# Kernel optimization log

Hardware: AMD Instinct MI355X
Metric: run time of the kernel (lower is better)

The kernel has to match this reference:

```python
import jax, jax.numpy as jnp
import numpy as np

N_NODES = 100000
IN_DIM = 64
OUT_DIM = 64
N_EDGES = 1250000


def setup_inputs() -> dict:
    key = jax.random.key(0)
    k1, k2, k3, k4 = jax.random.split(key, 4)
    x = jax.random.normal(k1, (N_NODES, IN_DIM), dtype=jnp.float32)
    edge_index = jax.random.randint(k2, (2, N_EDGES), 0, N_NODES, dtype=jnp.int32)
    # Linear weights stored as [in, out] so y = x @ W (equivalent to torch x @ W.T)
    s = 1.0 / np.sqrt(IN_DIM)
    W1 = jax.random.uniform(k3, (IN_DIM, OUT_DIM), dtype=jnp.float32, minval=-s, maxval=s)
    W2 = jax.random.uniform(k4, (IN_DIM, OUT_DIM), dtype=jnp.float32, minval=-s, maxval=s)
    return {"x": x, "edge_index": edge_index, "W1": W1, "W2": W2}


def reference(x, edge_index, W1, W2):
    # self part: [N, out]
    self_part = x @ W1
    # transform-then-gather is mathematically identical to gather-then-transform
    # (linear map commutes with row gather) and cheaper when E > N.
    msgs = (x @ W2)[edge_index[0]]            # [E, out]
    neighbor_part = jax.ops.segment_sum(msgs, edge_index[1], num_segments=x.shape[0])
    return jax.nn.relu(self_part + neighbor_part)
```

## Files before the change

### kernel.cpp

```cpp
#include <hip/hip_runtime.h>

#define N_NODES 100000
#define N_EDGES 1250000
#define DIM 64

#define B_SHIFT 7
#define BUCKET_NODES 128
#define NBUCKETS ((N_NODES + BUCKET_NODES - 1) / BUCKET_NODES)
#define CAP 2560
#define P_CHUNK 4096
#define P_THREADS 512
#define NBLK_P ((N_EDGES + P_CHUNK - 1) / P_CHUNK)
#define GEMM_BLOCKS 256
#define SG_THREADS 1024

typedef __attribute__((ext_vector_type(8))) short short8;
typedef __attribute__((ext_vector_type(4))) float f32x4;

static __host__ __device__ inline size_t align256(size_t x) { return (x + 255) & ~(size_t)255; }

__device__ inline float bf16_to_f32(unsigned short u) {
  return __uint_as_float(((unsigned)u) << 16);
}
__device__ inline unsigned short f32_to_bf16(float f) {
  unsigned u = __float_as_uint(f);
  u += 0x7FFFu + ((u >> 16) & 1u);
  return (unsigned short)(u >> 16);
}

__global__ __launch_bounds__(P_THREADS) void fused_gemm_partition(
    const float* __restrict__ x,
    const float* __restrict__ W1,
    const float* __restrict__ W2,
    unsigned short* __restrict__ y1b,
    unsigned short* __restrict__ y2b,
    const int* __restrict__ ei,
    int* __restrict__ gcursor,
    unsigned* __restrict__ pairs,
    int nTiles) {
  __shared__ int h[NBUCKETS];
  __shared__ int scn[NBUCKETS];
  __shared__ int cur[NBUCKETS];
  __shared__ int gbase[NBUCKETS];
  __shared__ int tsum[P_THREADS];
  __shared__ unsigned sval[P_CHUNK];
  __shared__ int saddr[P_CHUNK];

  if (blockIdx.x < NBLK_P) {
    const int nE = N_EDGES;
    int tid = threadIdx.x;
    int base = blockIdx.x * P_CHUNK;
    int end = min(base + P_CHUNK, nE);
    int cntE = end - base;

    for (int i = tid; i < NBUCKETS; i += P_THREADS) h[i] = 0;
    __syncthreads();
    for (int e = base + tid; e < end; e += P_THREADS)
      atomicAdd(&h[ei[nE + e] >> B_SHIFT], 1);
    __syncthreads();

    {
      int b0 = tid * 2;
      int l0 = 0, l1 = 0, s = 0;
      if (b0 < NBUCKETS)     { l0 = s; s += h[b0]; }
      if (b0 + 1 < NBUCKETS) { l1 = s; s += h[b0 + 1]; }
      tsum[tid] = s;
      __syncthreads();
      for (int off = 1; off < P_THREADS; off <<= 1) {
        int t = (tid >= off) ? tsum[tid - off] : 0;
        __syncthreads();
        tsum[tid] += t;
        __syncthreads();
      }
      int p = tsum[tid] - s;
      if (b0 < NBUCKETS)     scn[b0] = p + l0;
      if (b0 + 1 < NBUCKETS) scn[b0 + 1] = p + l1;
    }
    __syncthreads();

    for (int i = tid; i < NBUCKETS; i += P_THREADS) {
      int c = h[i];
      gbase[i] = c ? atomicAdd(&gcursor[i], c) : 0;
      cur[i] = scn[i];
    }
    __syncthreads();

    for (int e = base + tid; e < end; e += P_THREADS) {
      int dst = ei[nE + e];
      int src = ei[e];
      int b = dst >> B_SHIFT;
      int lp = atomicAdd(&cur[b], 1);
      int inb = lp - scn[b];
      int gpos = gbase[b] + inb;
      sval[lp] = (unsigned)src | ((unsigned)(dst & (BUCKET_NODES - 1)) << 17);
      saddr[lp] = (gpos < CAP) ? (b * CAP + gpos) : -1;
    }
    __syncthreads();

    for (int j = tid; j < cntE; j += P_THREADS) {
      int a = saddr[j];
      if (a >= 0) pairs[a] = sval[j];
    }
  } else {
    int lane = threadIdx.x & 63;
    int wave = ((blockIdx.x - NBLK_P) * P_THREADS + (int)threadIdx.x) >> 6;
    int nWaves = GEMM_BLOCKS * (P_THREADS / 64);
    int m = lane & 15;
    int q = lane >> 4;

    short8 wf[2][2][4];
#pragma unroll
    for (int w = 0; w < 2; ++w) {
      const float* W = w ? W2 : W1;
#pragma unroll
      for (int kh = 0; kh < 2; ++kh)
#pragma unroll
        for (int nt = 0; nt < 4; ++nt) {
          short8 f;
#pragma unroll
          for (int j = 0; j < 8; ++j) {
            int k = kh * 32 + q * 8 + j;
            f[j] = (short)f32_to_bf16(W[k * DIM + nt * 16 + m]);
          }
          wf[w][kh][nt] = f;
        }
    }

    for (int t = wave; t < nTiles; t += nWaves) {
      int rowBase = t * 16;
      const float* xr = x + (size_t)(rowBase + m) * DIM + q * 8;

      short8 af[2];
#pragma unroll
      for (int kh = 0; kh < 2; ++kh) {
        float4 u0 = *(const float4*)(xr + kh * 32);
        float4 u1 = *(const float4*)(xr + kh * 32 + 4);
        short8 f;
        f[0] = (short)f32_to_bf16(u0.x);
        f[1] = (short)f32_to_bf16(u0.y);
        f[2] = (short)f32_to_bf16(u0.z);
        f[3] = (short)f32_to_bf16(u0.w);
        f[4] = (short)f32_to_bf16(u1.x);
        f[5] = (short)f32_to_bf16(u1.y);
        f[6] = (short)f32_to_bf16(u1.z);
        f[7] = (short)f32_to_bf16(u1.w);
        af[kh] = f;
      }

#pragma unroll
      for (int w = 0; w < 2; ++w) {
        unsigned short* Y = w ? y2b : y1b;
        f32x4 acc[4];
#pragma unroll
        for (int nt = 0; nt < 4; ++nt) {
          acc[nt] = (f32x4){0.f, 0.f, 0.f, 0.f};
          acc[nt] = __builtin_amdgcn_mfma_f32_16x16x32_bf16(af[0], wf[w][0][nt], acc[nt], 0, 0, 0);
          acc[nt] = __builtin_amdgcn_mfma_f32_16x16x32_bf16(af[1], wf[w][1][nt], acc[nt], 0, 0, 0);
        }
#pragma unroll
        for (int nt = 0; nt < 4; ++nt)
#pragma unroll
          for (int r = 0; r < 4; ++r)
            Y[(size_t)(rowBase + q * 4 + r) * DIM + nt * 16 + m] = f32_to_bf16(acc[nt][r]);
      }
    }
  }
}

__global__ __launch_bounds__(SG_THREADS) void sort_gather(
    const unsigned* __restrict__ pairs,
    const int* __restrict__ gcursor,
    const unsigned short* __restrict__ y1b,
    const unsigned short* __restrict__ y2b,
    float* __restrict__ out,
    int nNodesTotal) {
  __shared__ unsigned buf[CAP];
  __shared__ unsigned sorted[CAP];
  __shared__ int cnt[BUCKET_NODES];
  __shared__ int scn[BUCKET_NODES];
  __shared__ int cur[BUCKET_NODES];

  int b = blockIdx.x;
  int n = min(gcursor[b], CAP);
  int tid = threadIdx.x;
  const unsigned* pb = pairs + (size_t)b * CAP;

  if (tid < BUCKET_NODES) cnt[tid] = 0;
  __syncthreads();
  for (int i = tid; i < n; i += SG_THREADS) {
    unsigned w = pb[i];
    buf[i] = w;
    atomicAdd(&cnt[(w >> 17) & 127], 1);
  }
  __syncthreads();

  if (tid < 64) {
    int b0 = tid * 2;
    int c0 = cnt[b0], c1 = cnt[b0 + 1];
    int s = c0 + c1;
#pragma unroll
    for (int off = 1; off < 64; off <<= 1) {
      int t = __shfl_up(s, off, 64);
      if (tid >= off) s += t;
    }
    scn[b0] = s - c1;
    scn[b0 + 1] = s;
    cur[b0] = s - c1 - c0;
    cur[b0 + 1] = s - c1;
  }
  __syncthreads();

  for (int i = tid; i < n; i += SG_THREADS) {
    unsigned w = buf[i];
    int l = (int)((w >> 17) & 127);
    int p = atomicAdd(&cur[l], 1);
    sorted[p] = w & 0x1FFFFu;
  }
  __syncthreads();

  int lane = tid & 63;
  int wv = tid >> 6;
  int g = lane >> 4;
  int c16 = lane & 15;
  const ushort4* y2q = (const ushort4*)y2b;
  const ushort4* y1q = (const ushort4*)y1b;
  int nodeBase = b << B_SHIFT;
  int numNodes = min(BUCKET_NODES, nNodesTotal - nodeBase);

  for (int ln = wv; ln < numNodes; ln += (SG_THREADS / 64)) {
    int deg = cnt[ln];
    int begin = scn[ln] - deg;
    int end = begin + deg;

    float ax = 0.f, ay = 0.f, az = 0.f, aw = 0.f;
    float bx = 0.f, by = 0.f, bz = 0.f, bw = 0.f;
    int e = begin;
    for (; e + 7 < end; e += 8) {
      int s0 = (int)sorted[e + g];
      int s1 = (int)sorted[e + 4 + g];
      ushort4 u0 = y2q[(size_t)s0 * 16 + c16];
      ushort4 u1 = y2q[(size_t)s1 * 16 + c16];
      ax += bf16_to_f32(u0.x); ay += bf16_to_f32(u0.y);
      az += bf16_to_f32(u0.z); aw += bf16_to_f32(u0.w);
      bx += bf16_to_f32(u1.x); by += bf16_to_f32(u1.y);
      bz += bf16_to_f32(u1.z); bw += bf16_to_f32(u1.w);
    }
    for (; e + 3 < end; e += 4) {
      int s = (int)sorted[e + g];
      ushort4 u = y2q[(size_t)s * 16 + c16];
      ax += bf16_to_f32(u.x); ay += bf16_to_f32(u.y);
      az += bf16_to_f32(u.z); aw += bf16_to_f32(u.w);
    }
    if (e + g < end) {
      int s = (int)sorted[e + g];
      ushort4 u = y2q[(size_t)s * 16 + c16];
      ax += bf16_to_f32(u.x); ay += bf16_to_f32(u.y);
      az += bf16_to_f32(u.z); aw += bf16_to_f32(u.w);
    }

    float sx = ax + bx, sy = ay + by, sz = az + bz, sw = aw + bw;
    sx += __shfl_xor(sx, 16, 64);
    sy += __shfl_xor(sy, 16, 64);
    sz += __shfl_xor(sz, 16, 64);
    sw += __shfl_xor(sw, 16, 64);
    sx += __shfl_xor(sx, 32, 64);
    sy += __shfl_xor(sy, 32, 64);
    sz += __shfl_xor(sz, 32, 64);
    sw += __shfl_xor(sw, 32, 64);

    if (lane < 16) {
      int node = nodeBase + ln;
      ushort4 s1v = y1q[(size_t)node * 16 + lane];
      float4 o;
      o.x = fmaxf(bf16_to_f32(s1v.x) + sx, 0.0f);
      o.y = fmaxf(bf16_to_f32(s1v.y) + sy, 0.0f);
      o.z = fmaxf(bf16_to_f32(s1v.z) + sz, 0.0f);
      o.w = fmaxf(bf16_to_f32(s1v.w) + sw, 0.0f);
      ((float4*)out)[(size_t)node * 16 + lane] = o;
    }
  }
}

__global__ __launch_bounds__(256) void gemm_simple(
    const float* __restrict__ x, const float* __restrict__ W1, const float* __restrict__ W2,
    float* __restrict__ y1, unsigned short* __restrict__ y2b, int n) {
  int row = blockIdx.x * blockDim.x + threadIdx.x;
  if (row >= n) return;
  float xv[DIM];
  const float4* xr = (const float4*)(x + (size_t)row * DIM);
#pragma unroll
  for (int i = 0; i < DIM / 4; ++i) {
    float4 t = xr[i];
    xv[4 * i] = t.x; xv[4 * i + 1] = t.y; xv[4 * i + 2] = t.z; xv[4 * i + 3] = t.w;
  }
#pragma unroll
  for (int m = 0; m < 2; ++m) {
    const float* W = (m == 0) ? W1 : W2;
#pragma unroll
    for (int cc = 0; cc < DIM; cc += 16) {
      float acc[16];
#pragma unroll
      for (int c2 = 0; c2 < 16; ++c2) acc[c2] = 0.0f;
      for (int k = 0; k < DIM; ++k) {
        float xk = xv[k];
        const float* wr = W + k * DIM + cc;
#pragma unroll
        for (int c2 = 0; c2 < 16; ++c2) acc[c2] = fmaf(xk, wr[c2], acc[c2]);
      }
      if (m == 0) {
        for (int c2 = 0; c2 < 16; ++c2) y1[(size_t)row * DIM + cc + c2] = acc[c2];
      } else {
        for (int c2 = 0; c2 < 16; ++c2) y2b[(size_t)row * DIM + cc + c2] = f32_to_bf16(acc[c2]);
      }
    }
  }
}

__global__ __launch_bounds__(256) void scatter_add(const int* __restrict__ ei,
                                                   const unsigned short* __restrict__ y2b,
                                                   float* __restrict__ out, int nE) {
  int gid = blockIdx.x * blockDim.x + threadIdx.x;
  int edge = gid >> 6;
  int lane = threadIdx.x & 63;
  if (edge >= nE) return;
  int src = __builtin_amdgcn_readfirstlane(ei[edge]);
  int dst = __builtin_amdgcn_readfirstlane(ei[nE + edge]);
  atomicAdd(&out[(size_t)dst * DIM + lane], bf16_to_f32(y2b[(size_t)src * DIM + lane]));
}

__global__ __launch_bounds__(256) void relu_inplace(float* __restrict__ out, int n4) {
  int i = blockIdx.x * blockDim.x + threadIdx.x;
  if (i >= n4) return;
  float4* p = (float4*)out;
  float4 v = p[i];
  v.x = fmaxf(v.x, 0.0f);
  v.y = fmaxf(v.y, 0.0f);
  v.z = fmaxf(v.z, 0.0f);
  v.w = fmaxf(v.w, 0.0f);
  p[i] = v;
}

extern "C" void kernel_launch(void* const* d_in, const int* in_sizes, int n_in,
                              void* d_out, int out_size, void* d_ws, size_t ws_size,
                              hipStream_t stream) {
  const float* x  = (const float*)d_in[0];
  const int*   ei = (const int*)d_in[1];
  const float* W1 = (const float*)d_in[2];
  const float* W2 = (const float*)d_in[3];
  float* out = (float*)d_out;

  char* ws = (char*)d_ws;
  size_t off = 0;
  unsigned short* y2b = (unsigned short*)(ws + off); off += align256((size_t)N_NODES * DIM * sizeof(unsigned short));
  unsigned short* y1b = (unsigned short*)(ws + off); off += align256((size_t)N_NODES * DIM * sizeof(unsigned short));
  int* gcursor = (int*)(ws + off);                   off += align256((size_t)NBUCKETS * sizeof(int));
  unsigned* pairs = (unsigned*)(ws + off);           off += align256((size_t)NBUCKETS * CAP * sizeof(unsigned));
  size_t required = off;

  if (ws_size >= required) {
    hipMemsetAsync(gcursor, 0, (size_t)NBUCKETS * sizeof(int), stream);
    fused_gemm_partition<<<NBLK_P + GEMM_BLOCKS, P_THREADS, 0, stream>>>(
        x, W1, W2, y1b, y2b, ei, gcursor, pairs, N_NODES / 16);
    sort_gather<<<NBUCKETS, SG_THREADS, 0, stream>>>(pairs, gcursor, y1b, y2b, out, N_NODES);
  } else {
    {
      int blocks = (N_NODES + 255) / 256;
      gemm_simple<<<blocks, 256, 0, stream>>>(x, W1, W2, out, y2b, N_NODES);
    }
    {
      long long threads = (long long)N_EDGES * 64;
      int blocks = (int)((threads + 255) / 256);
      scatter_add<<<blocks, 256, 0, stream>>>(ei, y2b, out, N_EDGES);
    }
    {
      int n4 = N_NODES * DIM / 4;
      int blocks = (n4 + 255) / 256;
      relu_inplace<<<blocks, 256, 0, stream>>>(out, n4);
    }
  }
}
```

Before: 147.3 us.

## Split fused GEMM/partition kernel and zero bucket cursors inside GEMM

Splits the combined GEMM+edge-partition kernel into two separate launches. The GEMM kernel zeroes the bucket cursors in block 0, which removes the hipMemsetAsync. The partition kernel uses smaller chunks (2048 edges, 256 threads), padded 1024-bin histograms and a shuffle-based wave prefix scan in place of the shared-memory Hillis-Steele scan. This lowers launch and scan overhead and shrinks the per-block LDS footprint, but the GEMM and partition work no longer overlap inside one launch.

```diff
diff --git a/kernel.cpp b/kernel.cpp
--- a/kernel.cpp
+++ b/kernel.cpp
@@ -7,11 +7,12 @@
 #define B_SHIFT 7
 #define BUCKET_NODES 128
 #define NBUCKETS ((N_NODES + BUCKET_NODES - 1) / BUCKET_NODES)
+#define NBINS 1024
 #define CAP 2560
-#define P_CHUNK 4096
-#define P_THREADS 512
+#define P_CHUNK 2048
+#define P_THREADS 256
 #define NBLK_P ((N_EDGES + P_CHUNK - 1) / P_CHUNK)
-#define GEMM_BLOCKS 256
+#define GEMM_BLOCKS 512
 #define SG_THREADS 1024
 
 typedef __attribute__((ext_vector_type(8))) short short8;
@@ -28,141 +29,147 @@
   return (unsigned short)(u >> 16);
 }
 
-__global__ __launch_bounds__(P_THREADS) void fused_gemm_partition(
+__global__ __launch_bounds__(P_THREADS) void partition_sorted(
+    const int* __restrict__ ei,
+    int* __restrict__ gcursor,
+    unsigned* __restrict__ pairs) {
+  __shared__ int h[NBINS];
+  __shared__ int scn[NBINS];
+  __shared__ int gbase[NBUCKETS];
+  __shared__ int wsum[4];
+  __shared__ unsigned sval[P_CHUNK];
+  __shared__ int saddr[P_CHUNK];
+
+  const int nE = N_EDGES;
+  int tid = threadIdx.x;
+  int base = blockIdx.x * P_CHUNK;
+  int end = min(base + P_CHUNK, nE);
+  int cntE = end - base;
+
+  for (int i = tid; i < NBINS; i += P_THREADS) h[i] = 0;
+  __syncthreads();
+  for (int e = base + tid; e < end; e += P_THREADS)
+    atomicAdd(&h[ei[nE + e] >> B_SHIFT], 1);
+  __syncthreads();
+
+  int b0 = tid * 4;
+  int c0 = h[b0], c1 = h[b0 + 1], c2 = h[b0 + 2], c3 = h[b0 + 3];
+  int s = c0 + c1 + c2 + c3;
+  int lane = tid & 63;
+  int wv = tid >> 6;
+  int ss = s;
+#pragma unroll
+  for (int off = 1; off < 64; off <<= 1) {
+    int t = __shfl_up(ss, off, 64);
+    if (lane >= off) ss += t;
+  }
+  if (lane == 63) wsum[wv] = ss;
+  __syncthreads();
+  int wpre = 0;
+#pragma unroll
+  for (int w = 0; w < 4; ++w) wpre += (w < wv) ? wsum[w] : 0;
+  int excl = wpre + ss - s;
+  scn[b0] = excl;
+  scn[b0 + 1] = excl + c0;
+  scn[b0 + 2] = excl + c0 + c1;
+  scn[b0 + 3] = excl + c0 + c1 + c2;
+#pragma unroll
+  for (int j = 0; j < 4; ++j) {
+    int b = b0 + j;
+    int c = (j == 0) ? c0 : (j == 1) ? c1 : (j == 2) ? c2 : c3;
+    if (b < NBUCKETS) gbase[b] = c ? atomicAdd(&gcursor[b], c) : 0;
+    h[b] = scn[b];
+  }
+  __syncthreads();
+
+  for (int e = base + tid; e < end; e += P_THREADS) {
+    int dst = ei[nE + e];
+    int src = ei[e];
+    int b = dst >> B_SHIFT;
+    int lp = atomicAdd(&h[b], 1);
+    int gpos = gbase[b] + (lp - scn[b]);
+    sval[lp] = (unsigned)src | ((unsigned)(dst & (BUCKET_NODES - 1)) << 17);
+    saddr[lp] = (gpos < CAP) ? (b * CAP + gpos) : -1;
+  }
+  __syncthreads();
+
+  for (int j = tid; j < cntE; j += P_THREADS) {
+    int a = saddr[j];
+    if (a >= 0) pairs[a] = sval[j];
+  }
+}
+
+__global__ __launch_bounds__(256) void gemm_mfma(
     const float* __restrict__ x,
     const float* __restrict__ W1,
     const float* __restrict__ W2,
     unsigned short* __restrict__ y1b,
     unsigned short* __restrict__ y2b,
-    const int* __restrict__ ei,
     int* __restrict__ gcursor,
-    unsigned* __restrict__ pairs,
     int nTiles) {
-  __shared__ int h[NBUCKETS];
-  __shared__ int scn[NBUCKETS];
-  __shared__ int cur[NBUCKETS];
-  __shared__ int gbase[NBUCKETS];
-  __shared__ int tsum[P_THREADS];
-  __shared__ unsigned sval[P_CHUNK];
-  __shared__ int saddr[P_CHUNK];
-
-  if (blockIdx.x < NBLK_P) {
-    const int nE = N_EDGES;
-    int tid = threadIdx.x;
-    int base = blockIdx.x * P_CHUNK;
-    int end = min(base + P_CHUNK, nE);
-    int cntE = end - base;
-
-    for (int i = tid; i < NBUCKETS; i += P_THREADS) h[i] = 0;
-    __syncthreads();
-    for (int e = base + tid; e < end; e += P_THREADS)
-      atomicAdd(&h[ei[nE + e] >> B_SHIFT], 1);
-    __syncthreads();
-
-    {
-      int b0 = tid * 2;
-      int l0 = 0, l1 = 0, s = 0;
-      if (b0 < NBUCKETS)     { l0 = s; s += h[b0]; }
-      if (b0 + 1 < NBUCKETS) { l1 = s; s += h[b0 + 1]; }
-      tsum[tid] = s;
-      __syncthreads();
-      for (int off = 1; off < P_THREADS; off <<= 1) {
-        int t = (tid >= off) ? tsum[tid - off] : 0;
-        __syncthreads();
-        tsum[tid] += t;
-        __syncthreads();
+  if (blockIdx.x == 0) {
+    for (int i = threadIdx.x; i < NBUCKETS; i += 256) gcursor[i] = 0;
+  }
+  int lane = threadIdx.x & 63;
+  int wave = (blockIdx.x * 256 + (int)threadIdx.x) >> 6;
+  int nWaves = GEMM_BLOCKS * 4;
+  int m = lane & 15;
+  int q = lane >> 4;
+
+  short8 wf[2][2][4];
+#pragma unroll
+  for (int w = 0; w < 2; ++w) {
+    const float* W = w ? W2 : W1;
+#pragma unroll
+    for (int kh = 0; kh < 2; ++kh)
+#pragma unroll
+      for (int nt = 0; nt < 4; ++nt) {
+        short8 f;
+#pragma unroll
+        for (int j = 0; j < 8; ++j) {
+          int k = kh * 32 + q * 8 + j;
+          f[j] = (short)f32_to_bf16(W[k * DIM + nt * 16 + m]);
+        }
+        wf[w][kh][nt] = f;
       }
-      int p = tsum[tid] - s;
-      if (b0 < NBUCKETS)     scn[b0] = p + l0;
-      if (b0 + 1 < NBUCKETS) scn[b0 + 1] = p + l1;
-    }
-    __syncthreads();
-
-    for (int i = tid; i < NBUCKETS; i += P_THREADS) {
-      int c = h[i];
-      gbase[i] = c ? atomicAdd(&gcursor[i], c) : 0;
-      cur[i] = scn[i];
-    }
-    __syncthreads();
-
-    for (int e = base + tid; e < end; e += P_THREADS) {
-      int dst = ei[nE + e];
-      int src = ei[e];
-      int b = dst >> B_SHIFT;
-      int lp = atomicAdd(&cur[b], 1);
-      int inb = lp - scn[b];
-      int gpos = gbase[b] + inb;
-      sval[lp] = (unsigned)src | ((unsigned)(dst & (BUCKET_NODES - 1)) << 17);
-      saddr[lp] = (gpos < CAP) ? (b * CAP + gpos) : -1;
-    }
-    __syncthreads();
-
-    for (int j = tid; j < cntE; j += P_THREADS) {
-      int a = saddr[j];
-      if (a >= 0) pairs[a] = sval[j];
-    }
-  } else {
-    int lane = threadIdx.x & 63;
-    int wave = ((blockIdx.x - NBLK_P) * P_THREADS + (int)threadIdx.x) >> 6;
-    int nWaves = GEMM_BLOCKS * (P_THREADS / 64);
-    int m = lane & 15;
-    int q = lane >> 4;
-
-    short8 wf[2][2][4];
+  }
+
+  for (int t = wave; t < nTiles; t += nWaves) {
+    int rowBase = t * 16;
+    const float* xr = x + (size_t)(rowBase + m) * DIM + q * 8;
+
+    short8 af[2];
+#pragma unroll
+    for (int kh = 0; kh < 2; ++kh) {
+      float4 u0 = *(const float4*)(xr + kh * 32);
+      float4 u1 = *(const float4*)(xr + kh * 32 + 4);
+      short8 f;
+      f[0] = (short)f32_to_bf16(u0.x);
+      f[1] = (short)f32_to_bf16(u0.y);
+      f[2] = (short)f32_to_bf16(u0.z);
+      f[3] = (short)f32_to_bf16(u0.w);
+      f[4] = (short)f32_to_bf16(u1.x);
+      f[5] = (short)f32_to_bf16(u1.y);
+      f[6] = (short)f32_to_bf16(u1.z);
+      f[7] = (short)f32_to_bf16(u1.w);
+      af[kh] = f;
+    }
+
 #pragma unroll
     for (int w = 0; w < 2; ++w) {
-      const float* W = w ? W2 : W1;
-#pragma unroll
-      for (int kh = 0; kh < 2; ++kh)
-#pragma unroll
-        for (int nt = 0; nt < 4; ++nt) {
-          short8 f;
-#pragma unroll
-          for (int j = 0; j < 8; ++j) {
-            int k = kh * 32 + q * 8 + j;
-            f[j] = (short)f32_to_bf16(W[k * DIM + nt * 16 + m]);
-          }
-          wf[w][kh][nt] = f;
-        }
-    }
-
-    for (int t = wave; t < nTiles; t += nWaves) {
-      int rowBase = t * 16;
-      const float* xr = x + (size_t)(rowBase + m) * DIM + q * 8;
-
-      short8 af[2];
-#pragma unroll
-      for (int kh = 0; kh < 2; ++kh) {
-        float4 u0 = *(const float4*)(xr + kh * 32);
-        float4 u1 = *(const float4*)(xr + kh * 32 + 4);
-        short8 f;
-        f[0] = (short)f32_to_bf16(u0.x);
-        f[1] = (short)f32_to_bf16(u0.y);
-        f[2] = (short)f32_to_bf16(u0.z);
-        f[3] = (short)f32_to_bf16(u0.w);
-        f[4] = (short)f32_to_bf16(u1.x);
-        f[5] = (short)f32_to_bf16(u1.y);
-        f[6] = (short)f32_to_bf16(u1.z);
-        f[7] = (short)f32_to_bf16(u1.w);
-        af[kh] = f;
+      unsigned short* Y = w ? y2b : y1b;
+      f32x4 acc[4];
+#pragma unroll
+      for (int nt = 0; nt < 4; ++nt) {
+        acc[nt] = (f32x4){0.f, 0.f, 0.f, 0.f};
+        acc[nt] = __builtin_amdgcn_mfma_f32_16x16x32_bf16(af[0], wf[w][0][nt], acc[nt], 0, 0, 0);
+        acc[nt] = __builtin_amdgcn_mfma_f32_16x16x32_bf16(af[1], wf[w][1][nt], acc[nt], 0, 0, 0);
       }
-
-#pragma unroll
-      for (int w = 0; w < 2; ++w) {
-        unsigned short* Y = w ? y2b : y1b;
-        f32x4 acc[4];
-#pragma unroll
-        for (int nt = 0; nt < 4; ++nt) {
-          acc[nt] = (f32x4){0.f, 0.f, 0.f, 0.f};
-          acc[nt] = __builtin_amdgcn_mfma_f32_16x16x32_bf16(af[0], wf[w][0][nt], acc[nt], 0, 0, 0);
-          acc[nt] = __builtin_amdgcn_mfma_f32_16x16x32_bf16(af[1], wf[w][1][nt], acc[nt], 0, 0, 0);
-        }
-#pragma unroll
-        for (int nt = 0; nt < 4; ++nt)
-#pragma unroll
-          for (int r = 0; r < 4; ++r)
-            Y[(size_t)(rowBase + q * 4 + r) * DIM + nt * 16 + m] = f32_to_bf16(acc[nt][r]);
-      }
+#pragma unroll
+      for (int nt = 0; nt < 4; ++nt)
+#pragma unroll
+        for (int r = 0; r < 4; ++r)
+          Y[(size_t)(rowBase + q * 4 + r) * DIM + nt * 16 + m] = f32_to_bf16(acc[nt][r]);
     }
   }
 }
@@ -358,9 +365,8 @@
   size_t required = off;
 
   if (ws_size >= required) {
-    hipMemsetAsync(gcursor, 0, (size_t)NBUCKETS * sizeof(int), stream);
-    fused_gemm_partition<<<NBLK_P + GEMM_BLOCKS, P_THREADS, 0, stream>>>(
-        x, W1, W2, y1b, y2b, ei, gcursor, pairs, N_NODES / 16);
+    gemm_mfma<<<GEMM_BLOCKS, 256, 0, stream>>>(x, W1, W2, y1b, y2b, gcursor, N_NODES / 16);
+    partition_sorted<<<NBLK_P, P_THREADS, 0, stream>>>(ei, gcursor, pairs);
     sort_gather<<<NBUCKETS, SG_THREADS, 0, stream>>>(pairs, gcursor, y1b, y2b, out, N_NODES);
   } else {
     {
```

Result: slower. 183.2 us (+24.3%).
